# Kernel tuning notes

Hardware: AMD Instinct MI355X
Metric: run time of the kernel (lower is better)

## Reference

```python
import jax, jax.numpy as jnp
import numpy as np

MARGIN = 0.3
EPS = 1e-8


def setup_inputs() -> dict:
    key = jax.random.key(0)
    k1, k2 = jax.random.split(key)
    B, D, NUM_IDS = 8192, 128, 1024
    embeddings = jax.random.normal(k1, (B, D), dtype=jnp.float32)
    labels = jax.random.randint(k2, (B,), 0, NUM_IDS, dtype=jnp.int64)
    return {"embeddings": embeddings, "labels": labels}


def _pairwise_distance(embeddings):
    # dist[i,j] = sqrt(relu(||e_i||^2 - 2 e_i.e_j + ||e_j||^2) + eps)
    dot = embeddings @ embeddings.T                       # [B, B]
    sq = jnp.diagonal(dot)                                # [B]
    d2 = sq[None, :] - 2.0 * dot + sq[:, None]
    return jnp.sqrt(jax.nn.relu(d2) + EPS)


def reference(embeddings, labels):
    B = labels.shape[0]
    dist = _pairwise_distance(embeddings)                 # [B, B]

    same = labels[:, None] == labels[None, :]             # [B, B]
    eye = jnp.eye(B, dtype=bool)
    pos_mask = same & ~eye
    neg_mask = ~same

    neg_inf = jnp.finfo(dist.dtype).min
    pos_inf = jnp.finfo(dist.dtype).max
    hardest_pos = jnp.max(jnp.where(pos_mask, dist, neg_inf), axis=1)  # [B]
    hardest_neg = jnp.min(jnp.where(neg_mask, dist, pos_inf), axis=1)  # [B]

    valid = pos_mask.any(axis=1) & neg_mask.any(axis=1)   # [B]
    per_anchor = jax.nn.relu(hardest_pos - hardest_neg + MARGIN)
    loss_sum = jnp.sum(jnp.where(valid, per_anchor, 0.0))
    n_triplets = jnp.sum(valid)
    return loss_sum / jnp.maximum(n_triplets, 1).astype(loss_sum.dtype)
```

## Files before the change

kernel.cpp:

```cpp
#include <hip/hip_runtime.h>

#define BSZ 8192
#define DIM 128
#define MARGIN 0.3f
#define EPS 1e-8f
#define NJ 32
#define JCHUNK 256
#define NPH 8

typedef __bf16 bf16x8 __attribute__((ext_vector_type(8)));
typedef float f32x4 __attribute__((ext_vector_type(4)));

#define AS1 __attribute__((address_space(1)))
#define AS3 __attribute__((address_space(3)))

__device__ __forceinline__ unsigned enc_ord(float f) {
    unsigned u = __float_as_uint(f);
    return (u & 0x80000000u) ? ~u : (u | 0x80000000u);
}
__device__ __forceinline__ float dec_ord(unsigned e) {
    unsigned u = (e & 0x80000000u) ? (e & 0x7FFFFFFFu) : ~e;
    return __uint_as_float(u);
}


__global__ __launch_bounds__(256) void k_prep(const float* __restrict__ emb,
                                              __bf16* __restrict__ hi,
                                              float* __restrict__ sq,
                                              unsigned* __restrict__ maxp,
                                              unsigned* __restrict__ minn,
                                              float* __restrict__ sumcnt) {
    int row = blockIdx.x * 4 + (threadIdx.x >> 6);
    int lane = threadIdx.x & 63;
    float2 v = *(const float2*)&emb[(size_t)row * DIM + lane * 2];
    union { __bf16 b[2]; unsigned u; } p;
    p.b[0] = (__bf16)v.x;
    p.b[1] = (__bf16)v.y;
    ((unsigned*)hi)[row * 64 + lane] = p.u;
    float s = v.x * v.x + v.y * v.y;
#pragma unroll
    for (int m = 32; m >= 1; m >>= 1) s += __shfl_xor(s, m);
    if (lane == 0) {
        sq[row] = s;
        maxp[row] = 0u;
        minn[row] = 0xFFFFFFFFu;
    }
    if (blockIdx.x == 0 && threadIdx.x == 0) {
        sumcnt[0] = 0.0f;
        ((unsigned*)sumcnt)[1] = 0u;
    }
}

__global__ __launch_bounds__(256, 4) void k_mfma(const __bf16* __restrict__ hi,
                                                 const int* __restrict__ labels,
                                                 const float* __restrict__ sq,
                                                 unsigned* __restrict__ maxp,
                                                 unsigned* __restrict__ minn) {
    __shared__ char Bst[2][8][1024];
    __shared__ float sqlds[JCHUNK];
    __shared__ int lablds[JCHUNK];

    const int tid = threadIdx.x;
    const int lane = tid & 63;
    const int wave = tid >> 6;
    const int lr = lane & 15;
    const int lq = lane >> 4;
    const int it0 = blockIdx.x * 128 + wave * 32;
    const int it1 = it0 + 16;
    const int j0 = blockIdx.y * JCHUNK;
    const float INF = __uint_as_float(0x7F800000u);

    sqlds[tid] = sq[j0 + tid];
    lablds[tid] = labels[j0 + tid];

    bf16x8 a0[4], a1[4];
    const __bf16* ap = hi + (size_t)(it0 + lr) * DIM + lq * 8;
#pragma unroll
    for (int f = 0; f < 4; ++f) {
        a0[f] = *(const bf16x8*)&ap[f * 32];
        a1[f] = *(const bf16x8*)&ap[16 * DIM + f * 32];
        asm volatile("" : "+v"(a0[f]));
        asm volatile("" : "+v"(a1[f]));
    }
    const int4 li0 = *(const int4*)&labels[it0 + lq * 4];
    const int4 li1 = *(const int4*)&labels[it1 + lq * 4];
    const int labi0[4] = {li0.x, li0.y, li0.z, li0.w};
    const int labi1[4] = {li1.x, li1.y, li1.z, li1.w};

    float mp0[4], mp1[4], mn0[4], mn1[4];
#pragma unroll
    for (int r = 0; r < 4; ++r) {
        mp0[r] = -INF; mp1[r] = -INF;
        mn0[r] = INF;  mn1[r] = INF;
    }

    const int m0 = wave * 2, m1 = m0 + 1;
    const __bf16* bsA = hi + (size_t)(j0 + (m0 >> 2) * 16 + lr) * DIM + (m0 & 3) * 32 + lq * 8;
    const __bf16* bsB = hi + (size_t)(j0 + (m1 >> 2) * 16 + lr) * DIM + (m1 & 3) * 32 + lq * 8;
#define STAGE(t, buf)                                                              \
    do {                                                                           \
        __builtin_amdgcn_global_load_lds(                                          \
            (const AS1 void*)(bsA + (size_t)(t) * 32 * DIM),                       \
            (AS3 void*)&Bst[buf][m0][0], 16, 0, 0);                                \
        __builtin_amdgcn_global_load_lds(                                          \
            (const AS1 void*)(bsB + (size_t)(t) * 32 * DIM),                       \
            (AS3 void*)&Bst[buf][m1][0], 16, 0, 0);                                \
    } while (0)

    STAGE(0, 0);
    __syncthreads();

#pragma unroll 1
    for (int t = 0; t < NPH; ++t) {
        if (t + 1 < NPH) STAGE(t + 1, (t + 1) & 1);

        const float sqj0 = sqlds[t * 32 + lr];
        const float sqj1 = sqlds[t * 32 + 16 + lr];
        const int labj0 = lablds[t * 32 + lr];
        const int labj1 = lablds[t * 32 + 16 + lr];

        const bf16x8* bp = (const bf16x8*)&Bst[t & 1][0][0];
        f32x4 acc00 = {0, 0, 0, 0}, acc01 = {0, 0, 0, 0};
        f32x4 acc10 = {0, 0, 0, 0}, acc11 = {0, 0, 0, 0};
#pragma unroll
        for (int f = 0; f < 4; ++f) {
            bf16x8 b0 = bp[f * 64 + lane];
            bf16x8 b1 = bp[(4 + f) * 64 + lane];
            acc00 = __builtin_amdgcn_mfma_f32_16x16x32_bf16(a0[f], b0, acc00, 0, 0, 0);
            acc10 = __builtin_amdgcn_mfma_f32_16x16x32_bf16(a1[f], b0, acc10, 0, 0, 0);
            acc01 = __builtin_amdgcn_mfma_f32_16x16x32_bf16(a0[f], b1, acc01, 0, 0, 0);
            acc11 = __builtin_amdgcn_mfma_f32_16x16x32_bf16(a1[f], b1, acc11, 0, 0, 0);
        }

#pragma unroll
        for (int r = 0; r < 4; ++r) {
            float k00 = fmaf(-2.0f, acc00[r], sqj0);
            float k01 = fmaf(-2.0f, acc01[r], sqj1);
            float k10 = fmaf(-2.0f, acc10[r], sqj0);
            float k11 = fmaf(-2.0f, acc11[r], sqj1);
            bool s00 = (labj0 == labi0[r]);
            bool s01 = (labj1 == labi0[r]);
            bool s10 = (labj0 == labi1[r]);
            bool s11 = (labj1 == labi1[r]);
            mp0[r] = s00 ? fmaxf(mp0[r], k00) : mp0[r];
            mn0[r] = s00 ? mn0[r] : fminf(mn0[r], k00);
            mp0[r] = s01 ? fmaxf(mp0[r], k01) : mp0[r];
            mn0[r] = s01 ? mn0[r] : fminf(mn0[r], k01);
            mp1[r] = s10 ? fmaxf(mp1[r], k10) : mp1[r];
            mn1[r] = s10 ? mn1[r] : fminf(mn1[r], k10);
            mp1[r] = s11 ? fmaxf(mp1[r], k11) : mp1[r];
            mn1[r] = s11 ? mn1[r] : fminf(mn1[r], k11);
        }

        __syncthreads();
    }
#undef STAGE

#pragma unroll
    for (int m = 1; m < 16; m <<= 1) {
#pragma unroll
        for (int r = 0; r < 4; ++r) {
            mp0[r] = fmaxf(mp0[r], __shfl_xor(mp0[r], m));
            mn0[r] = fminf(mn0[r], __shfl_xor(mn0[r], m));
            mp1[r] = fmaxf(mp1[r], __shfl_xor(mp1[r], m));
            mn1[r] = fminf(mn1[r], __shfl_xor(mn1[r], m));
        }
    }
    if (lr == 0) {
#pragma unroll
        for (int r = 0; r < 4; ++r) {
            atomicMax(&maxp[it0 + lq * 4 + r], enc_ord(mp0[r]));
            atomicMin(&minn[it0 + lq * 4 + r], enc_ord(mn0[r]));
            atomicMax(&maxp[it1 + lq * 4 + r], enc_ord(mp1[r]));
            atomicMin(&minn[it1 + lq * 4 + r], enc_ord(mn1[r]));
        }
    }
}

__global__ __launch_bounds__(256) void k_final(const unsigned* __restrict__ maxp,
                                               const unsigned* __restrict__ minn,
                                               const float* __restrict__ sq,
                                               float* __restrict__ sumcnt) {
    int i = blockIdx.x * 256 + threadIdx.x;
    float mpd = dec_ord(maxp[i]);
    float mnd = dec_ord(minn[i]);
    float sqi = sq[i];
    bool valid = (mpd > -1e30f) && (mnd < 1e30f);
    float hp = sqrtf(fmaxf(sqi + mpd, 0.0f) + EPS);
    float hn = sqrtf(fmaxf(sqi + mnd, 0.0f) + EPS);
    float per = valid ? fmaxf(hp - hn + MARGIN, 0.0f) : 0.0f;
    unsigned cnt = valid ? 1u : 0u;
#pragma unroll
    for (int m = 32; m >= 1; m >>= 1) {
        per += __shfl_xor(per, m);
        cnt += __shfl_xor(cnt, m);
    }
    __shared__ float ssum[4];
    __shared__ unsigned scnt[4];
    int wid = threadIdx.x >> 6;
    if ((threadIdx.x & 63) == 0) { ssum[wid] = per; scnt[wid] = cnt; }
    __syncthreads();
    if (threadIdx.x == 0) {
        float s = ssum[0] + ssum[1] + ssum[2] + ssum[3];
        unsigned c = scnt[0] + scnt[1] + scnt[2] + scnt[3];
        atomicAdd(&sumcnt[0], s);
        atomicAdd((unsigned*)&sumcnt[1], c);
    }
}

__global__ void k_out(const float* __restrict__ sumcnt, float* __restrict__ out) {
    if (threadIdx.x == 0) {
        float s = sumcnt[0];
        unsigned c = ((const unsigned*)sumcnt)[1];
        out[0] = s / (float)(c > 0u ? c : 1u);
    }
}

extern "C" void kernel_launch(void* const* d_in, const int* in_sizes, int n_in,
                              void* d_out, int out_size, void* d_ws, size_t ws_size,
                              hipStream_t stream) {
    const float* emb    = (const float*)d_in[0];
    const int*   labels = (const int*)d_in[1];

    __bf16* hi = (__bf16*)d_ws;
    float*  sq = (float*)(hi + (size_t)BSZ * DIM);
    unsigned* maxp = (unsigned*)(sq + BSZ);
    unsigned* minn = maxp + BSZ;
    float* sumcnt = (float*)(minn + BSZ);
    float* out = (float*)d_out;

    k_prep<<<dim3(BSZ / 4), dim3(256), 0, stream>>>(emb, hi, sq, maxp, minn, sumcnt);
    k_mfma<<<dim3(BSZ / 128, NJ), dim3(256), 0, stream>>>(hi, labels, sq, maxp, minn);
    k_final<<<dim3(BSZ / 256), dim3(256), 0, stream>>>(maxp, minn, sq, sumcnt);
    k_out<<<dim3(1), dim3(64), 0, stream>>>(sumcnt, out);
}
```

Measured before the change: 49.05 us.

## Sort rows by label so off-block tiles skip positive-mask epilogue; deepen staging

Adds a counting-sort pass (histogram, prefix scan, atomic scatter) that permutes embeddings and labels so rows with equal labels sit next to each other. Each block then computes which 32-column phases can hold same-label columns and runs only a cheaper negative-min epilogue everywhere else. The B-tile staging also moves from a 2-deep to a 4-deep LDS ring with explicit vmcnt waits and raw barriers. The cost is two extra small kernel launches, including a single-block sort, plus the permutation gather. Order-insensitive reductions keep the result unchanged.

```diff
diff --git a/kernel.cpp b/kernel.cpp
--- a/kernel.cpp
+++ b/kernel.cpp
@@ -2,6 +2,7 @@
 
 #define BSZ 8192
 #define DIM 128
+#define NLAB 1024
 #define MARGIN 0.3f
 #define EPS 1e-8f
 #define NJ 32
@@ -23,8 +24,48 @@
     return __uint_as_float(u);
 }
 
+template <int N>
+__device__ __forceinline__ void waitv() {
+    if constexpr (N == 4) asm volatile("s_waitcnt vmcnt(4)" ::: "memory");
+    else if constexpr (N == 2) asm volatile("s_waitcnt vmcnt(2)" ::: "memory");
+    else asm volatile("s_waitcnt vmcnt(0)" ::: "memory");
+}
+
+__global__ __launch_bounds__(1024) void k_sort(const int* __restrict__ labels,
+                                               unsigned* __restrict__ start,
+                                               unsigned* __restrict__ offset) {
+    __shared__ unsigned h[NLAB];
+    const int tid = threadIdx.x;
+    h[tid] = 0u;
+    __syncthreads();
+#pragma unroll
+    for (int s = 0; s < BSZ / NLAB; ++s)
+        atomicAdd(&h[labels[s * NLAB + tid]], 1u);
+    __syncthreads();
+    for (int d = 1; d < NLAB; d <<= 1) {
+        unsigned w = (tid >= d) ? h[tid - d] : 0u;
+        __syncthreads();
+        h[tid] += w;
+        __syncthreads();
+    }
+    start[tid + 1] = h[tid];
+    if (tid == 0) start[0] = 0u;
+    offset[tid] = (tid > 0) ? h[tid - 1] : 0u;
+}
+
+__global__ __launch_bounds__(256) void k_scatter(const int* __restrict__ labels,
+                                                 unsigned* __restrict__ offset,
+                                                 int* __restrict__ perm,
+                                                 int* __restrict__ slab) {
+    int i = blockIdx.x * 256 + threadIdx.x;
+    int lab = labels[i];
+    unsigned pos = atomicAdd(&offset[lab], 1u);
+    perm[pos] = i;
+    slab[pos] = lab;
+}
 
 __global__ __launch_bounds__(256) void k_prep(const float* __restrict__ emb,
+                                              const int* __restrict__ perm,
                                               __bf16* __restrict__ hi,
                                               float* __restrict__ sq,
                                               unsigned* __restrict__ maxp,
@@ -32,7 +73,8 @@
                                               float* __restrict__ sumcnt) {
     int row = blockIdx.x * 4 + (threadIdx.x >> 6);
     int lane = threadIdx.x & 63;
-    float2 v = *(const float2*)&emb[(size_t)row * DIM + lane * 2];
+    int src = perm[row];
+    float2 v = *(const float2*)&emb[(size_t)src * DIM + lane * 2];
     union { __bf16 b[2]; unsigned u; } p;
     p.b[0] = (__bf16)v.x;
     p.b[1] = (__bf16)v.y;
@@ -52,11 +94,12 @@
 }
 
 __global__ __launch_bounds__(256, 4) void k_mfma(const __bf16* __restrict__ hi,
-                                                 const int* __restrict__ labels,
+                                                 const int* __restrict__ slab,
+                                                 const unsigned* __restrict__ startp,
                                                  const float* __restrict__ sq,
                                                  unsigned* __restrict__ maxp,
                                                  unsigned* __restrict__ minn) {
-    __shared__ char Bst[2][8][1024];
+    __shared__ char Bst[4][8][1024];
     __shared__ float sqlds[JCHUNK];
     __shared__ int lablds[JCHUNK];
 
@@ -65,13 +108,25 @@
     const int wave = tid >> 6;
     const int lr = lane & 15;
     const int lq = lane >> 4;
-    const int it0 = blockIdx.x * 128 + wave * 32;
+    const int i0 = blockIdx.x * 128;
+    const int it0 = i0 + wave * 32;
     const int it1 = it0 + 16;
     const int j0 = blockIdx.y * JCHUNK;
     const float INF = __uint_as_float(0x7F800000u);
 
+    const int lf = slab[i0];
+    const int ll = slab[i0 + 127];
+    const int blo = (int)startp[lf];
+    const int bhi = (int)startp[ll + 1];
+    unsigned mmask = 0;
+#pragma unroll
+    for (int tt = 0; tt < NPH; ++tt) {
+        int c0 = j0 + tt * 32;
+        if (bhi > c0 && blo < c0 + 32) mmask |= (1u << tt);
+    }
+
     sqlds[tid] = sq[j0 + tid];
-    lablds[tid] = labels[j0 + tid];
+    lablds[tid] = slab[j0 + tid];
 
     bf16x8 a0[4], a1[4];
     const __bf16* ap = hi + (size_t)(it0 + lr) * DIM + lq * 8;
@@ -82,8 +137,8 @@
         asm volatile("" : "+v"(a0[f]));
         asm volatile("" : "+v"(a1[f]));
     }
-    const int4 li0 = *(const int4*)&labels[it0 + lq * 4];
-    const int4 li1 = *(const int4*)&labels[it1 + lq * 4];
+    const int4 li0 = *(const int4*)&slab[it0 + lq * 4];
+    const int4 li1 = *(const int4*)&slab[it1 + lq * 4];
     const int labi0[4] = {li0.x, li0.y, li0.z, li0.w};
     const int labi1[4] = {li1.x, li1.y, li1.z, li1.w};
 
@@ -108,18 +163,22 @@
     } while (0)
 
     STAGE(0, 0);
+    STAGE(1, 1);
     __syncthreads();
 
 #pragma unroll 1
     for (int t = 0; t < NPH; ++t) {
-        if (t + 1 < NPH) STAGE(t + 1, (t + 1) & 1);
+        if (t + 2 < NPH) STAGE(t + 2, (t + 2) & 3);
+        if (t < NPH - 2) waitv<4>();
+        else if (t == NPH - 2) waitv<2>();
+        else waitv<0>();
+        __builtin_amdgcn_s_barrier();
+        __builtin_amdgcn_sched_barrier(0);
 
         const float sqj0 = sqlds[t * 32 + lr];
         const float sqj1 = sqlds[t * 32 + 16 + lr];
-        const int labj0 = lablds[t * 32 + lr];
-        const int labj1 = lablds[t * 32 + 16 + lr];
-
-        const bf16x8* bp = (const bf16x8*)&Bst[t & 1][0][0];
+
+        const bf16x8* bp = (const bf16x8*)&Bst[t & 3][0][0];
         f32x4 acc00 = {0, 0, 0, 0}, acc01 = {0, 0, 0, 0};
         f32x4 acc10 = {0, 0, 0, 0}, acc11 = {0, 0, 0, 0};
 #pragma unroll
@@ -132,27 +191,39 @@
             acc11 = __builtin_amdgcn_mfma_f32_16x16x32_bf16(a1[f], b1, acc11, 0, 0, 0);
         }
 
-#pragma unroll
-        for (int r = 0; r < 4; ++r) {
-            float k00 = fmaf(-2.0f, acc00[r], sqj0);
-            float k01 = fmaf(-2.0f, acc01[r], sqj1);
-            float k10 = fmaf(-2.0f, acc10[r], sqj0);
-            float k11 = fmaf(-2.0f, acc11[r], sqj1);
-            bool s00 = (labj0 == labi0[r]);
-            bool s01 = (labj1 == labi0[r]);
-            bool s10 = (labj0 == labi1[r]);
-            bool s11 = (labj1 == labi1[r]);
-            mp0[r] = s00 ? fmaxf(mp0[r], k00) : mp0[r];
-            mn0[r] = s00 ? mn0[r] : fminf(mn0[r], k00);
-            mp0[r] = s01 ? fmaxf(mp0[r], k01) : mp0[r];
-            mn0[r] = s01 ? mn0[r] : fminf(mn0[r], k01);
-            mp1[r] = s10 ? fmaxf(mp1[r], k10) : mp1[r];
-            mn1[r] = s10 ? mn1[r] : fminf(mn1[r], k10);
-            mp1[r] = s11 ? fmaxf(mp1[r], k11) : mp1[r];
-            mn1[r] = s11 ? mn1[r] : fminf(mn1[r], k11);
+        if (mmask & (1u << t)) {
+            const int labj0 = lablds[t * 32 + lr];
+            const int labj1 = lablds[t * 32 + 16 + lr];
+#pragma unroll
+            for (int r = 0; r < 4; ++r) {
+                float k00 = fmaf(-2.0f, acc00[r], sqj0);
+                float k01 = fmaf(-2.0f, acc01[r], sqj1);
+                float k10 = fmaf(-2.0f, acc10[r], sqj0);
+                float k11 = fmaf(-2.0f, acc11[r], sqj1);
+                bool s00 = (labj0 == labi0[r]);
+                bool s01 = (labj1 == labi0[r]);
+                bool s10 = (labj0 == labi1[r]);
+                bool s11 = (labj1 == labi1[r]);
+                mp0[r] = s00 ? fmaxf(mp0[r], k00) : mp0[r];
+                mn0[r] = s00 ? mn0[r] : fminf(mn0[r], k00);
+                mp0[r] = s01 ? fmaxf(mp0[r], k01) : mp0[r];
+                mn0[r] = s01 ? mn0[r] : fminf(mn0[r], k01);
+                mp1[r] = s10 ? fmaxf(mp1[r], k10) : mp1[r];
+                mn1[r] = s10 ? mn1[r] : fminf(mn1[r], k10);
+                mp1[r] = s11 ? fmaxf(mp1[r], k11) : mp1[r];
+                mn1[r] = s11 ? mn1[r] : fminf(mn1[r], k11);
+            }
+        } else {
+#pragma unroll
+            for (int r = 0; r < 4; ++r) {
+                float k00 = fmaf(-2.0f, acc00[r], sqj0);
+                float k01 = fmaf(-2.0f, acc01[r], sqj1);
+                float k10 = fmaf(-2.0f, acc10[r], sqj0);
+                float k11 = fmaf(-2.0f, acc11[r], sqj1);
+                mn0[r] = fminf(fminf(mn0[r], k00), k01);
+                mn1[r] = fminf(fminf(mn1[r], k10), k11);
+            }
         }
-
-        __syncthreads();
     }
 #undef STAGE
 
@@ -222,15 +293,22 @@
     const float* emb    = (const float*)d_in[0];
     const int*   labels = (const int*)d_in[1];
 
-    __bf16* hi = (__bf16*)d_ws;
-    float*  sq = (float*)(hi + (size_t)BSZ * DIM);
-    unsigned* maxp = (unsigned*)(sq + BSZ);
-    unsigned* minn = maxp + BSZ;
-    float* sumcnt = (float*)(minn + BSZ);
-    float* out = (float*)d_out;
-
-    k_prep<<<dim3(BSZ / 4), dim3(256), 0, stream>>>(emb, hi, sq, maxp, minn, sumcnt);
-    k_mfma<<<dim3(BSZ / 128, NJ), dim3(256), 0, stream>>>(hi, labels, sq, maxp, minn);
+    float* wsf = (float*)d_ws;
+    __bf16*   hi     = (__bf16*)wsf;
+    float*    sq     = wsf + 524288;
+    unsigned* maxp   = (unsigned*)(wsf + 532480);
+    unsigned* minn   = (unsigned*)(wsf + 540672);
+    float*    sumcnt = wsf + 548864;
+    unsigned* start  = (unsigned*)(wsf + 548868);
+    unsigned* offset = (unsigned*)(wsf + 549896);
+    int*      perm   = (int*)(wsf + 550920);
+    int*      slab   = (int*)(wsf + 559112);
+    float*    out    = (float*)d_out;
+
+    k_sort<<<dim3(1), dim3(1024), 0, stream>>>(labels, start, offset);
+    k_scatter<<<dim3(BSZ / 256), dim3(256), 0, stream>>>(labels, offset, perm, slab);
+    k_prep<<<dim3(BSZ / 4), dim3(256), 0, stream>>>(emb, perm, hi, sq, maxp, minn, sumcnt);
+    k_mfma<<<dim3(BSZ / 128, NJ), dim3(256), 0, stream>>>(hi, slab, start, sq, maxp, minn);
     k_final<<<dim3(BSZ / 256), dim3(256), 0, stream>>>(maxp, minn, sq, sumcnt);
     k_out<<<dim3(1), dim3(64), 0, stream>>>(sumcnt, out);
 }
```

New measurement: 53.63 us. +9.3%, slower.
